# Kernel tuning notes

Hardware: AMD Instinct MI355X
Metric: run time of the kernel (lower is better)

Reference implementation:

```python
import jax, jax.numpy as jnp
import numpy as np

N, T, LH, HEADS, C, E = 100000, 24, 64, 4, 16, 1600000
NEG_SLOPE = 0.2  # PyG GATConv leaky_relu slope


def setup_inputs() -> dict:
    key = jax.random.key(0)
    ks = jax.random.split(key, 24)
    s = 0.05
    inp = {
        'input_tensor': jax.random.normal(ks[0], (N, T), jnp.float32),
        'edge_index': jax.random.randint(ks[1], (2, E), 0, N, jnp.int32),
        'edge_attr': jax.random.uniform(ks[2], (E, 1), jnp.float32),
        'knn_mask_short': jax.random.randint(ks[3], (E,), 0, 2, jnp.int32).astype(bool),
        # LSTM layer 1 (input_size=1): gate order i,f,g,o
        'W_ih1': jax.random.normal(ks[4], (4 * LH, 1), jnp.float32) * s,
        'W_hh1': jax.random.normal(ks[5], (4 * LH, LH), jnp.float32) * s,
        'b_ih1': jax.random.normal(ks[6], (4 * LH,), jnp.float32) * s,
        'b_hh1': jax.random.normal(ks[7], (4 * LH,), jnp.float32) * s,
        # LSTM layer 2 (input_size=LH)
        'W_ih2': jax.random.normal(ks[8], (4 * LH, LH), jnp.float32) * s,
        'W_hh2': jax.random.normal(ks[9], (4 * LH, LH), jnp.float32) * s,
        'b_ih2': jax.random.normal(ks[10], (4 * LH,), jnp.float32) * s,
        'b_hh2': jax.random.normal(ks[11], (4 * LH,), jnp.float32) * s,
        # GATConv params
        'gat_lin_w': jax.random.normal(ks[12], (HEADS * C, LH), jnp.float32) * s,
        'gat_lin_edge_w': jax.random.normal(ks[13], (HEADS * C, 1), jnp.float32) * s,
        'att_src': jax.random.normal(ks[14], (HEADS, C), jnp.float32) * s,
        'att_dst': jax.random.normal(ks[15], (HEADS, C), jnp.float32) * s,
        'att_edge': jax.random.normal(ks[16], (HEADS, C), jnp.float32) * s,
        'gat_bias': jax.random.normal(ks[17], (HEADS * C,), jnp.float32) * s,
        # final Linear
        'fc_w': jax.random.normal(ks[18], (1, HEADS * C), jnp.float32) * s,
        'fc_b': jax.random.normal(ks[19], (1,), jnp.float32) * s,
    }
    return inp


def _lstm_cell(x, h, c, W_ih, W_hh, b):
    z = x @ W_ih.T + h @ W_hh.T + b  # (N, 4H)
    i, f, g, o = jnp.split(z, 4, axis=-1)
    c = jax.nn.sigmoid(f) * c + jax.nn.sigmoid(i) * jnp.tanh(g)
    h = jax.nn.sigmoid(o) * jnp.tanh(c)
    return h, c


def reference(input_tensor, edge_index, edge_attr, knn_mask_short,
              W_ih1, W_hh1, b_ih1, b_hh1, W_ih2, W_hh2, b_ih2, b_hh2,
              gat_lin_w, gat_lin_edge_w, att_src, att_dst, att_edge, gat_bias,
              fc_w, fc_b):
    n = input_tensor.shape[0]
    # --- 2-layer LSTM over time, fused per-step (only final h2 needed) ---
    xs = input_tensor.T[:, :, None]  # (T, N, 1)
    b1 = b_ih1 + b_hh1
    b2 = b_ih2 + b_hh2
    z = jnp.zeros((n, LH), input_tensor.dtype)

    def step(carry, x_t):
        h1, c1, h2, c2 = carry
        h1, c1 = _lstm_cell(x_t, h1, c1, W_ih1, W_hh1, b1)
        h2, c2 = _lstm_cell(h1, h2, c2, W_ih2, W_hh2, b2)
        return (h1, c1, h2, c2), None

    (h1, c1, h2, c2), _ = jax.lax.scan(step, (z, z, z, z), xs)
    lstm_out = h2  # (N, LH): last time-step output of layer 2

    # --- GATConv (heads concat, edge_dim=1), eval mode (dropout off) ---
    x = (lstm_out @ gat_lin_w.T).reshape(n, HEADS, C)  # (N, H, C)
    a_src = jnp.einsum('nhc,hc->nh', x, att_src)
    a_dst = jnp.einsum('nhc,hc->nh', x, att_dst)
    src, dst = edge_index[0], edge_index[1]
    e = (edge_attr @ gat_lin_edge_w.T).reshape(-1, HEADS, C)  # (E, H, C)
    a_edge = jnp.einsum('ehc,hc->eh', e, att_edge)
    alpha = jax.nn.leaky_relu(a_src[src] + a_dst[dst] + a_edge, NEG_SLOPE)  # (E, H)
    # mask out non-'short' edges (equivalent to slicing them away)
    alpha = jnp.where(knn_mask_short[:, None], alpha, -1e30)
    amax = jax.ops.segment_max(alpha, dst, num_segments=n)  # (N, H)
    ex = jnp.exp(alpha - amax[dst]) * knn_mask_short[:, None].astype(alpha.dtype)
    denom = jax.ops.segment_sum(ex, dst, num_segments=n)  # (N, H)
    w = ex / jnp.maximum(denom[dst], 1e-16)  # (E, H) attention weights
    msg = x[src] * w[:, :, None]  # (E, H, C)
    out = jax.ops.segment_sum(msg, dst, num_segments=n).reshape(n, HEADS * C) + gat_bias

    out = jax.nn.elu(out)
    y = out @ fc_w.T + fc_b  # (N, 1)
    return y.reshape(n)
```

## Files before the change

kernel.cpp:

```cpp
#include <hip/hip_runtime.h>
#include <hip/hip_bf16.h>

#define T_STEPS 24
#define NSLOPE 0.2f
#define PITCH2 136
#define LOG2E 1.4426950408889634f

typedef _Float16 half8 __attribute__((ext_vector_type(8)));
typedef _Float16 half4_t __attribute__((ext_vector_type(4)));
typedef float floatx4 __attribute__((ext_vector_type(4)));

#if __has_builtin(__builtin_amdgcn_exp2f)
#define EXP2(x) __builtin_amdgcn_exp2f(x)
#else
#define EXP2(x) exp2f(x)
#endif
#define RCP(x) __builtin_amdgcn_rcpf(x)

#define ACT(A0,A1,A2,A3,CS,HP) {                                        \
    float i_ = RCP(1.f + EXP2(-(A0)));                                  \
    float f_ = RCP(1.f + EXP2(-(A1)));                                  \
    float gr = RCP(1.f + EXP2(-(A2)));                                  \
    float o_ = RCP(1.f + EXP2(-(A3)));                                  \
    float gs = fmaf(gr, 4.f*LOG2E, -2.f*LOG2E);                         \
    float cs = fmaf(f_, (CS), i_*gs);                                   \
    (CS) = cs;                                                          \
    float tc = fmaf(RCP(1.f + EXP2(-cs)), 2.f, -1.f);                   \
    (HP) = (_Float16)(o_*tc); }

__global__ __launch_bounds__(256) void prep_kernel(
    const float* __restrict__ W_ih1, const float* __restrict__ W_hh1,
    const float* __restrict__ b_ih1, const float* __restrict__ b_hh1,
    const float* __restrict__ W_ih2, const float* __restrict__ W_hh2,
    const float* __restrict__ b_ih2, const float* __restrict__ b_hh2,
    const float* __restrict__ glw, const float* __restrict__ glew,
    const float* __restrict__ atte, const unsigned char* __restrict__ mask_bytes,
    _Float16* __restrict__ W1F, _Float16* __restrict__ W2F, _Float16* __restrict__ W3F,
    float* __restrict__ b2P, float* __restrict__ ke, int* __restrict__ flag)
{
    int tid = blockIdx.x*blockDim.x + threadIdx.x;
    int nth = gridDim.x*blockDim.x;
    for (int idx = tid; idx < 24576; idx += nth){
        int b = idx & 7;
        int lane = (idx >> 3) & 63;
        int t2 = idx >> 9;
        int kt = t2 % 3;
        int t3 = t2 / 3;
        int m = t3 & 1, w = t3 >> 1;
        int row16 = lane & 15;
        int g = row16 & 3, cl = row16 >> 2;
        int row = g*64 + 8*w + 4*m + cl;
        float sc = (g == 2) ? 2.f*LOG2E : LOG2E;
        int k = (lane>>4)*8 + b;
        float val;
        if (kt < 2){ val = W_hh1[row*64 + 32*kt + k]; }
        else { val = (k == 0) ? W_ih1[row] : (k == 1) ? (b_ih1[row]+b_hh1[row]) : 0.f; }
        W1F[idx] = (_Float16)(val * sc);
    }
    for (int idx = tid; idx < 32768; idx += nth){
        int b = idx & 7;
        int lane = (idx >> 3) & 63;
        int kt = (idx >> 9) & 3;
        int t3 = idx >> 11;
        int m = t3 & 1, w = t3 >> 1;
        int row16 = lane & 15;
        int g = row16 & 3, cl = row16 >> 2;
        int row = g*64 + 8*w + 4*m + cl;
        float sc = (g == 2) ? 2.f*LOG2E : LOG2E;
        int k = 32*kt + (lane>>4)*8 + b;
        W2F[idx] = (_Float16)(((k < 64) ? W_ih2[row*64 + k] : W_hh2[row*64 + (k-64)]) * sc);
    }
    for (int idx = tid; idx < 4096; idx += nth){
        int b = idx & 7, t1 = idx >> 3; int lane = t1 & 63, t2 = t1 >> 6;
        int kt = t2 & 1, w = t2 >> 1;
        int row = 16*w + (lane & 15);
        W3F[idx] = (_Float16)glw[row*64 + 32*kt + (lane>>4)*8 + b];
    }
    for (int idx = tid; idx < 4096; idx += nth){
        int r = idx & 3;
        int lane = (idx >> 2) & 63;
        int m = (idx >> 8) & 1;
        int w = idx >> 9;
        int grp = lane >> 4;
        int row = r*64 + 8*w + 4*m + grp;
        float sc = (r == 2) ? 2.f*LOG2E : LOG2E;
        b2P[idx] = (b_ih2[row] + b_hh2[row]) * sc;
    }
    if (tid < 4){ float s = 0.f; for (int c = 0; c < 16; c++) s += atte[tid*16+c]*glew[tid*16+c]; ke[tid] = s; }
    if (tid == 0){ int nz = 0;
        for (int i = 0; i < 4096; i++){ if ((i&3) != 0 && mask_bytes[i] != 0) nz++; }
        *flag = (nz == 0) ? 1 : 0; }
}

__global__ __launch_bounds__(256) void count_kernel(
    const int* __restrict__ ei, const void* __restrict__ maskp, const int* __restrict__ flag,
    int* __restrict__ deg, int E)
{
    int e = blockIdx.x*256 + threadIdx.x;
    if (e >= E) return;
    bool m = (*flag) ? (((const int*)maskp)[e] != 0) : (((const unsigned char*)maskp)[e] != 0);
    if (!m) return;
    atomicAdd(deg + ei[E + e], 1);
}

__global__ __launch_bounds__(1024) void scan_kernel(
    const int* __restrict__ deg, int* __restrict__ offs, int* __restrict__ cursor, int nn)
{
    __shared__ int wsum[16];
    __shared__ int sbase;
    int lane = threadIdx.x & 63, wv = threadIdx.x >> 6;
    if (threadIdx.x == 0) sbase = 0;
    __syncthreads();
    for (int base = 0; base < nn; base += 4096){
        int i0 = base + (int)threadIdx.x*4;
        int4 v = make_int4(0,0,0,0);
        if (i0 + 3 < nn) v = *(const int4*)(deg + i0);
        else {
            if (i0   < nn) v.x = deg[i0];
            if (i0+1 < nn) v.y = deg[i0+1];
            if (i0+2 < nn) v.z = deg[i0+2];
            if (i0+3 < nn) v.w = deg[i0+3];
        }
        int s = v.x + v.y + v.z + v.w;
        int sc = s;
        #pragma unroll
        for (int o = 1; o < 64; o <<= 1){ int t = __shfl_up(sc, o); if (lane >= o) sc += t; }
        if (lane == 63) wsum[wv] = sc;
        __syncthreads();
        int wbase = 0, total = 0;
        #pragma unroll
        for (int k = 0; k < 16; k++){ int sk = wsum[k]; if (k < wv) wbase += sk; total += sk; }
        int excl = sbase + wbase + sc - s;
        if (i0 < nn){
            int e0 = excl, e1 = e0 + v.x, e2 = e1 + v.y, e3 = e2 + v.z;
            if (i0 + 3 < nn){
                *(int4*)(offs + i0)   = make_int4(e0,e1,e2,e3);
                *(int4*)(cursor + i0) = make_int4(e0,e1,e2,e3);
            } else {
                offs[i0] = e0; cursor[i0] = e0;
                if (i0+1 < nn){ offs[i0+1] = e1; cursor[i0+1] = e1; }
                if (i0+2 < nn){ offs[i0+2] = e2; cursor[i0+2] = e2; }
            }
        }
        __syncthreads();
        if (threadIdx.x == 0) sbase += total;
        __syncthreads();
    }
    if (threadIdx.x == 0) offs[nn] = sbase;
}

__global__ __launch_bounds__(256) void scatter_kernel(
    const int* __restrict__ ei, const float* __restrict__ ea, const void* __restrict__ maskp,
    const int* __restrict__ flag, int* __restrict__ cursor, int2* __restrict__ rec, int E)
{
    int e = blockIdx.x*256 + threadIdx.x;
    if (e >= E) return;
    bool m = (*flag) ? (((const int*)maskp)[e] != 0) : (((const unsigned char*)maskp)[e] != 0);
    if (!m) return;
    int d = ei[E + e];
    int pos = atomicAdd(cursor + d, 1);
    rec[pos] = make_int2(ei[e], __float_as_int(ea[e]));
}

#define MFMA16(A,B,C) __builtin_amdgcn_mfma_f32_16x16x32_f16((A),(B),(C),0,0,0)

__device__ __forceinline__ void lstm_step(
    const _Float16* RB, _Float16* WB, const _Float16* x_lds, int t,
    const half8 (&w1f)[2][3], const half8 (&w2f)[2][4], const floatx4 (&b2v)[2],
    float* c1s, float* c2s, int col, int grp, int wv)
{
    #pragma unroll
    for (int nt = 0; nt < 2; nt++){
        int node = nt*16 + col;
        half8 bf0 = *(const half8*)&RB[node*PITCH2 + grp*8];
        half8 bf1 = *(const half8*)&RB[node*PITCH2 + 32 + grp*8];
        half8 xb;
        #pragma unroll
        for (int b = 0; b < 8; b++) xb[b] = (_Float16)0.f;
        _Float16 xv = x_lds[node*26 + t];
        if (grp == 0){ xb[0] = xv; xb[1] = (_Float16)1.0f; }
        floatx4 aA = {0,0,0,0}, aB = {0,0,0,0};
        aA = MFMA16(w1f[0][0], bf0, aA);  aB = MFMA16(w1f[1][0], bf0, aB);
        aA = MFMA16(w1f[0][1], bf1, aA);  aB = MFMA16(w1f[1][1], bf1, aB);
        aA = MFMA16(w1f[0][2], xb,  aA);  aB = MFMA16(w1f[1][2], xb,  aB);
        _Float16 hA, hB;
        ACT(aA[0], aA[1], aA[2], aA[3], c1s[nt*2+0], hA);
        ACT(aB[0], aB[1], aB[2], aB[3], c1s[nt*2+1], hB);
        WB[node*PITCH2 + 8*wv + grp]     = hA;
        WB[node*PITCH2 + 8*wv + 4 + grp] = hB;
    }
    __syncthreads();
    #pragma unroll
    for (int nt = 0; nt < 2; nt++){
        int node = nt*16 + col;
        half8 bf0 = *(const half8*)&WB[node*PITCH2 + grp*8];
        half8 bf1 = *(const half8*)&WB[node*PITCH2 + 32 + grp*8];
        half8 bf2 = *(const half8*)&RB[node*PITCH2 + 64 + grp*8];
        half8 bf3 = *(const half8*)&RB[node*PITCH2 + 96 + grp*8];
        floatx4 aA = b2v[0], aB = b2v[1];
        aA = MFMA16(w2f[0][0], bf0, aA);  aB = MFMA16(w2f[1][0], bf0, aB);
        aA = MFMA16(w2f[0][1], bf1, aA);  aB = MFMA16(w2f[1][1], bf1, aB);
        aA = MFMA16(w2f[0][2], bf2, aA);  aB = MFMA16(w2f[1][2], bf2, aB);
        aA = MFMA16(w2f[0][3], bf3, aA);  aB = MFMA16(w2f[1][3], bf3, aB);
        _Float16 hA, hB;
        ACT(aA[0], aA[1], aA[2], aA[3], c2s[nt*2+0], hA);
        ACT(aB[0], aB[1], aB[2], aB[3], c2s[nt*2+1], hB);
        WB[node*PITCH2 + 64 + 8*wv + grp]     = hA;
        WB[node*PITCH2 + 64 + 8*wv + 4 + grp] = hB;
    }
    __syncthreads();
}

__global__ __launch_bounds__(512) void lstm_kernel(
    const float* __restrict__ x_in,
    const _Float16* __restrict__ W1F, const _Float16* __restrict__ W2F, const _Float16* __restrict__ W3F,
    const float* __restrict__ b2P,
    const float* __restrict__ atts, const float* __restrict__ attd,
    float* __restrict__ x_out, float* __restrict__ a_src, float* __restrict__ a_dst, int nn)
{
    __shared__ _Float16 hbuf0[32*PITCH2];
    __shared__ _Float16 hbuf1[32*PITCH2];
    __shared__ _Float16 x_lds[32*26];

    const int wv   = threadIdx.x >> 6;
    const int lane = threadIdx.x & 63;
    const int grp  = lane >> 4;
    const int col  = lane & 15;
    const int node0 = blockIdx.x * 32;

    for (int i = threadIdx.x; i < 32*T_STEPS; i += 512){
        int node = i / T_STEPS, t = i % T_STEPS;
        int nd = node0 + node;
        x_lds[node*26 + t] = (_Float16)((nd < nn) ? x_in[nd*T_STEPS + t] : 0.f);
    }
    for (int i = threadIdx.x; i < 32*PITCH2/2; i += 512) ((float*)hbuf0)[i] = 0.f;

    const half8* W1Fv = (const half8*)W1F;
    const half8* W2Fv = (const half8*)W2F;
    half8 w1f[2][3], w2f[2][4];
    floatx4 b2v[2];
    #pragma unroll
    for (int m = 0; m < 2; m++){
        #pragma unroll
        for (int kt = 0; kt < 3; kt++) w1f[m][kt] = W1Fv[((wv*2+m)*3+kt)*64 + lane];
        #pragma unroll
        for (int kt = 0; kt < 4; kt++) w2f[m][kt] = W2Fv[((wv*2+m)*4+kt)*64 + lane];
        b2v[m] = *(const floatx4*)&b2P[((wv*2+m)*64 + lane)*4];
    }

    float c1s[4], c2s[4];
    #pragma unroll
    for (int i = 0; i < 4; i++){ c1s[i] = 0.f; c2s[i] = 0.f; }

    __syncthreads();

    for (int t = 0; t < T_STEPS; t += 2){
        lstm_step(hbuf0, hbuf1, x_lds, t,   w1f, w2f, b2v, c1s, c2s, col, grp, wv);
        lstm_step(hbuf1, hbuf0, x_lds, t+1, w1f, w2f, b2v, c1s, c2s, col, grp, wv);
    }

    if (wv < 4){
        const half8* W3Fv = (const half8*)W3F;
        half8 w3f0 = W3Fv[(wv*2+0)*64 + lane];
        half8 w3f1 = W3Fv[(wv*2+1)*64 + lane];
        float asw[4], adw[4];
        #pragma unroll
        for (int r = 0; r < 4; r++){ int ch = 16*wv + grp*4 + r; asw[r] = atts[ch]; adw[r] = attd[ch]; }
        #pragma unroll
        for (int nt = 0; nt < 2; nt++){
            int node = nt*16 + col;
            int nd = node0 + node;
            floatx4 pa = {0,0,0,0};
            half8 bf0 = *(const half8*)&hbuf0[node*PITCH2 + 64 + grp*8];
            half8 bf1 = *(const half8*)&hbuf0[node*PITCH2 + 96 + grp*8];
            pa = MFMA16(w3f0, bf0, pa);
            pa = MFMA16(w3f1, bf1, pa);
            float s  = pa[0]*asw[0] + pa[1]*asw[1] + pa[2]*asw[2] + pa[3]*asw[3];
            float dv = pa[0]*adw[0] + pa[1]*adw[1] + pa[2]*adw[2] + pa[3]*adw[3];
            s  += __shfl_xor(s, 16);  s  += __shfl_xor(s, 32);
            dv += __shfl_xor(dv, 16); dv += __shfl_xor(dv, 32);
            if (nd < nn){
                *(float4*)(x_out + (size_t)nd*64 + 16*wv + grp*4) = make_float4(pa[0], pa[1], pa[2], pa[3]);
                if (grp == 0) a_src[nd*4 + wv] = s;
                else if (grp == 1) a_dst[nd*4 + wv] = dv;
            }
        }
    }
}

__global__ __launch_bounds__(256) void gather_kernel(
    const int2* __restrict__ rec, const int* __restrict__ offs,
    const float* __restrict__ a_src, const float* __restrict__ a_dst, const float* __restrict__ ke,
    const float* __restrict__ xf, const float* __restrict__ gbias,
    const float* __restrict__ fcw, const float* __restrict__ fcb,
    float* __restrict__ y, int nn)
{
    int wv = threadIdx.x >> 6, lane = threadIdx.x & 63;
    int node = blockIdx.x*4 + wv;
    if (node >= nn) return;
    int h = lane >> 4;
    float keh = ke[h];
    float adv = a_dst[4*node + h];
    int beg = offs[node], end = offs[node+1];
    float acc = 0.f, dacc = 0.f;
    int j = beg;
    for (; j + 1 < end; j += 2){
        int2 r0 = rec[j], r1 = rec[j+1];
        int s0 = r0.x, s1 = r1.x;
        float as0 = a_src[4*s0 + h], as1 = a_src[4*s1 + h];
        float x0 = xf[(size_t)s0*64 + lane], x1 = xf[(size_t)s1*64 + lane];
        float a0 = as0 + adv + __int_as_float(r0.y)*keh;
        float a1 = as1 + adv + __int_as_float(r1.y)*keh;
        a0 = a0 > 0.f ? a0 : NSLOPE*a0;
        a1 = a1 > 0.f ? a1 : NSLOPE*a1;
        float e0 = __expf(a0), e1 = __expf(a1);
        dacc += e0 + e1;
        acc = fmaf(e0, x0, acc);
        acc = fmaf(e1, x1, acc);
    }
    if (j < end){
        int2 r = rec[j];
        int s = r.x;
        float a = a_src[4*s + h] + adv + __int_as_float(r.y)*keh;
        a = a > 0.f ? a : NSLOPE*a;
        float ev = __expf(a);
        dacc += ev;
        acc = fmaf(ev, xf[(size_t)s*64 + lane], acc);
    }
    float v = acc * RCP(fmaxf(dacc, 1e-16f)) + gbias[lane];
    v = v > 0.f ? v : (__expf(v) - 1.f);
    float r2 = v * fcw[lane];
    #pragma unroll
    for (int off = 1; off < 64; off <<= 1) r2 += __shfl_xor(r2, off, 64);
    if (lane == 0) y[node] = r2 + fcb[0];
}

extern "C" void kernel_launch(void* const* d_in, const int* in_sizes, int n_in,
                              void* d_out, int out_size, void* d_ws, size_t ws_size,
                              hipStream_t stream)
{
    const float* x_in  = (const float*)d_in[0];
    const int*   ei    = (const int*)d_in[1];
    const float* ea    = (const float*)d_in[2];
    const void*  mask  = d_in[3];
    const float* W_ih1 = (const float*)d_in[4];
    const float* W_hh1 = (const float*)d_in[5];
    const float* b_ih1 = (const float*)d_in[6];
    const float* b_hh1 = (const float*)d_in[7];
    const float* W_ih2 = (const float*)d_in[8];
    const float* W_hh2 = (const float*)d_in[9];
    const float* b_ih2 = (const float*)d_in[10];
    const float* b_hh2 = (const float*)d_in[11];
    const float* glw   = (const float*)d_in[12];
    const float* glew  = (const float*)d_in[13];
    const float* atts  = (const float*)d_in[14];
    const float* attd  = (const float*)d_in[15];
    const float* atte  = (const float*)d_in[16];
    const float* gbias = (const float*)d_in[17];
    const float* fcw   = (const float*)d_in[18];
    const float* fcb   = (const float*)d_in[19];

    const int NN = in_sizes[0] / T_STEPS;
    const int E  = in_sizes[1] / 2;

    float* ws = (float*)d_ws;
    size_t o = 0;
    _Float16* W1F = (_Float16*)(ws + o); o += 24576/2;
    _Float16* W2F = (_Float16*)(ws + o); o += 32768/2;
    _Float16* W3F = (_Float16*)(ws + o); o += 4096/2;
    float* b2P = ws + o; o += 4096;
    float* ke  = ws + o; o += 64;
    int*  flag = (int*)(ws + o); o += 64;
    float* asrc= ws + o; o += (size_t)NN*4;
    float* adst= ws + o; o += (size_t)NN*4;
    float* xf  = ws + o; o += (size_t)NN*64;
    int* deg    = (int*)(ws + o); o += NN;
    int* offs   = (int*)(ws + o); o += NN + 64;
    int* cursor = (int*)(ws + o); o += NN;
    int2* rec   = (int2*)(ws + o); o += (size_t)E*2;

    hipMemsetAsync(deg, 0, (size_t)NN*sizeof(int), stream);

    prep_kernel<<<64, 256, 0, stream>>>(W_ih1, W_hh1, b_ih1, b_hh1, W_ih2, W_hh2, b_ih2, b_hh2,
                                        glw, glew, atte, (const unsigned char*)mask,
                                        W1F, W2F, W3F, b2P, ke, flag);
    count_kernel<<<(E + 255)/256, 256, 0, stream>>>(ei, mask, flag, deg, E);
    scan_kernel<<<1, 1024, 0, stream>>>(deg, offs, cursor, NN);
    scatter_kernel<<<(E + 255)/256, 256, 0, stream>>>(ei, ea, mask, flag, cursor, rec, E);
    lstm_kernel<<<(NN + 31)/32, 512, 0, stream>>>(x_in, W1F, W2F, W3F, b2P,
                                                  atts, attd, xf, asrc, adst, NN);
    gather_kernel<<<(NN + 3)/4, 256, 0, stream>>>(rec, offs, asrc, adst, ke, xf,
                                                  gbias, fcw, fcb, (float*)d_out, NN);
}
```

Before: 625.1 us.

## Skew LSTM layers into a wavefront pipeline with one barrier per step

```diff
diff --git a/kernel.cpp b/kernel.cpp
--- a/kernel.cpp
+++ b/kernel.cpp
@@ -7,7 +7,7 @@
 #define LOG2E 1.4426950408889634f
 
 typedef _Float16 half8 __attribute__((ext_vector_type(8)));
-typedef _Float16 half4_t __attribute__((ext_vector_type(4)));
+typedef _Float16 half2_t __attribute__((ext_vector_type(2)));
 typedef float floatx4 __attribute__((ext_vector_type(4)));
 
 #if __has_builtin(__builtin_amdgcn_exp2f)
@@ -27,6 +27,8 @@
     (CS) = cs;                                                          \
     float tc = fmaf(RCP(1.f + EXP2(-cs)), 2.f, -1.f);                   \
     (HP) = (_Float16)(o_*tc); }
+
+#define MFMA16(A,B,C) __builtin_amdgcn_mfma_f32_16x16x32_f16((A),(B),(C),0,0,0)
 
 __global__ __launch_bounds__(256) void prep_kernel(
     const float* __restrict__ W_ih1, const float* __restrict__ W_hh1,
@@ -49,7 +51,7 @@
         int m = t3 & 1, w = t3 >> 1;
         int row16 = lane & 15;
         int g = row16 & 3, cl = row16 >> 2;
-        int row = g*64 + 8*w + 4*m + cl;
+        int row = g*64 + 8*w + 2*cl + m;
         float sc = (g == 2) ? 2.f*LOG2E : LOG2E;
         int k = (lane>>4)*8 + b;
         float val;
@@ -65,7 +67,7 @@
         int m = t3 & 1, w = t3 >> 1;
         int row16 = lane & 15;
         int g = row16 & 3, cl = row16 >> 2;
-        int row = g*64 + 8*w + 4*m + cl;
+        int row = g*64 + 8*w + 2*cl + m;
         float sc = (g == 2) ? 2.f*LOG2E : LOG2E;
         int k = 32*kt + (lane>>4)*8 + b;
         W2F[idx] = (_Float16)(((k < 64) ? W_ih2[row*64 + k] : W_hh2[row*64 + (k-64)]) * sc);
@@ -82,7 +84,7 @@
         int m = (idx >> 8) & 1;
         int w = idx >> 9;
         int grp = lane >> 4;
-        int row = r*64 + 8*w + 4*m + grp;
+        int row = r*64 + 8*w + 2*grp + m;
         float sc = (r == 2) ? 2.f*LOG2E : LOG2E;
         b2P[idx] = (b_ih2[row] + b_hh2[row]) * sc;
     }
@@ -162,51 +164,94 @@
     rec[pos] = make_int2(ei[e], __float_as_int(ea[e]));
 }
 
-#define MFMA16(A,B,C) __builtin_amdgcn_mfma_f32_16x16x32_f16((A),(B),(C),0,0,0)
-
-__device__ __forceinline__ void lstm_step(
-    const _Float16* RB, _Float16* WB, const _Float16* x_lds, int t,
+__device__ __forceinline__ void lstm_phase(
+    _Float16* A, _Float16* B, const _Float16* x_lds, int tn,
     const half8 (&w1f)[2][3], const half8 (&w2f)[2][4], const floatx4 (&b2v)[2],
     float* c1s, float* c2s, int col, int grp, int wv)
 {
     #pragma unroll
     for (int nt = 0; nt < 2; nt++){
         int node = nt*16 + col;
-        half8 bf0 = *(const half8*)&RB[node*PITCH2 + grp*8];
-        half8 bf1 = *(const half8*)&RB[node*PITCH2 + 32 + grp*8];
+        half8 h1a = *(const half8*)&A[node*PITCH2 + grp*8];
+        half8 h1b = *(const half8*)&A[node*PITCH2 + 32 + grp*8];
+        half8 h2a = *(const half8*)&B[node*PITCH2 + 64 + grp*8];
+        half8 h2b = *(const half8*)&B[node*PITCH2 + 96 + grp*8];
+        floatx4 aA = b2v[0], aB = b2v[1];
+        aA = MFMA16(w2f[0][0], h1a, aA);  aB = MFMA16(w2f[1][0], h1a, aB);
+        aA = MFMA16(w2f[0][1], h1b, aA);  aB = MFMA16(w2f[1][1], h1b, aB);
+        aA = MFMA16(w2f[0][2], h2a, aA);  aB = MFMA16(w2f[1][2], h2a, aB);
+        aA = MFMA16(w2f[0][3], h2b, aA);  aB = MFMA16(w2f[1][3], h2b, aB);
         half8 xb;
         #pragma unroll
         for (int b = 0; b < 8; b++) xb[b] = (_Float16)0.f;
-        _Float16 xv = x_lds[node*26 + t];
+        _Float16 xv = x_lds[node*26 + tn];
         if (grp == 0){ xb[0] = xv; xb[1] = (_Float16)1.0f; }
-        floatx4 aA = {0,0,0,0}, aB = {0,0,0,0};
-        aA = MFMA16(w1f[0][0], bf0, aA);  aB = MFMA16(w1f[1][0], bf0, aB);
-        aA = MFMA16(w1f[0][1], bf1, aA);  aB = MFMA16(w1f[1][1], bf1, aB);
-        aA = MFMA16(w1f[0][2], xb,  aA);  aB = MFMA16(w1f[1][2], xb,  aB);
-        _Float16 hA, hB;
-        ACT(aA[0], aA[1], aA[2], aA[3], c1s[nt*2+0], hA);
-        ACT(aB[0], aB[1], aB[2], aB[3], c1s[nt*2+1], hB);
-        WB[node*PITCH2 + 8*wv + grp]     = hA;
-        WB[node*PITCH2 + 8*wv + 4 + grp] = hB;
-    }
-    __syncthreads();
-    #pragma unroll
-    for (int nt = 0; nt < 2; nt++){
-        int node = nt*16 + col;
-        half8 bf0 = *(const half8*)&WB[node*PITCH2 + grp*8];
-        half8 bf1 = *(const half8*)&WB[node*PITCH2 + 32 + grp*8];
-        half8 bf2 = *(const half8*)&RB[node*PITCH2 + 64 + grp*8];
-        half8 bf3 = *(const half8*)&RB[node*PITCH2 + 96 + grp*8];
-        floatx4 aA = b2v[0], aB = b2v[1];
-        aA = MFMA16(w2f[0][0], bf0, aA);  aB = MFMA16(w2f[1][0], bf0, aB);
-        aA = MFMA16(w2f[0][1], bf1, aA);  aB = MFMA16(w2f[1][1], bf1, aB);
-        aA = MFMA16(w2f[0][2], bf2, aA);  aB = MFMA16(w2f[1][2], bf2, aB);
-        aA = MFMA16(w2f[0][3], bf3, aA);  aB = MFMA16(w2f[1][3], bf3, aB);
+        floatx4 cA = {0,0,0,0}, cB = {0,0,0,0};
+        cA = MFMA16(w1f[0][0], h1a, cA);  cB = MFMA16(w1f[1][0], h1a, cB);
+        cA = MFMA16(w1f[0][1], h1b, cA);  cB = MFMA16(w1f[1][1], h1b, cB);
+        cA = MFMA16(w1f[0][2], xb,  cA);  cB = MFMA16(w1f[1][2], xb,  cB);
         _Float16 hA, hB;
         ACT(aA[0], aA[1], aA[2], aA[3], c2s[nt*2+0], hA);
         ACT(aB[0], aB[1], aB[2], aB[3], c2s[nt*2+1], hB);
-        WB[node*PITCH2 + 64 + 8*wv + grp]     = hA;
-        WB[node*PITCH2 + 64 + 8*wv + 4 + grp] = hB;
+        { half2_t hh; hh[0] = hA; hh[1] = hB;
+          *(half2_t*)&A[node*PITCH2 + 64 + 8*wv + 2*grp] = hh; }
+        ACT(cA[0], cA[1], cA[2], cA[3], c1s[nt*2+0], hA);
+        ACT(cB[0], cB[1], cB[2], cB[3], c1s[nt*2+1], hB);
+        { half2_t hh; hh[0] = hA; hh[1] = hB;
+          *(half2_t*)&B[node*PITCH2 + 8*wv + 2*grp] = hh; }
+    }
+    __syncthreads();
+}
+
+__device__ __forceinline__ void lstm_l1only(
+    const _Float16* R, _Float16* W, const _Float16* x_lds,
+    const half8 (&w1f)[2][3], float* c1s, int col, int grp, int wv)
+{
+    #pragma unroll
+    for (int nt = 0; nt < 2; nt++){
+        int node = nt*16 + col;
+        half8 h1a = *(const half8*)&R[node*PITCH2 + grp*8];
+        half8 h1b = *(const half8*)&R[node*PITCH2 + 32 + grp*8];
+        half8 xb;
+        #pragma unroll
+        for (int b = 0; b < 8; b++) xb[b] = (_Float16)0.f;
+        _Float16 xv = x_lds[node*26 + 0];
+        if (grp == 0){ xb[0] = xv; xb[1] = (_Float16)1.0f; }
+        floatx4 cA = {0,0,0,0}, cB = {0,0,0,0};
+        cA = MFMA16(w1f[0][0], h1a, cA);  cB = MFMA16(w1f[1][0], h1a, cB);
+        cA = MFMA16(w1f[0][1], h1b, cA);  cB = MFMA16(w1f[1][1], h1b, cB);
+        cA = MFMA16(w1f[0][2], xb,  cA);  cB = MFMA16(w1f[1][2], xb,  cB);
+        _Float16 hA, hB;
+        ACT(cA[0], cA[1], cA[2], cA[3], c1s[nt*2+0], hA);
+        ACT(cB[0], cB[1], cB[2], cB[3], c1s[nt*2+1], hB);
+        half2_t hh; hh[0] = hA; hh[1] = hB;
+        *(half2_t*)&W[node*PITCH2 + 8*wv + 2*grp] = hh;
+    }
+    __syncthreads();
+}
+
+__device__ __forceinline__ void lstm_l2only(
+    _Float16* H1, const _Float16* H2,
+    const half8 (&w2f)[2][4], const floatx4 (&b2v)[2],
+    float* c2s, int col, int grp, int wv)
+{
+    #pragma unroll
+    for (int nt = 0; nt < 2; nt++){
+        int node = nt*16 + col;
+        half8 h1a = *(const half8*)&H1[node*PITCH2 + grp*8];
+        half8 h1b = *(const half8*)&H1[node*PITCH2 + 32 + grp*8];
+        half8 h2a = *(const half8*)&H2[node*PITCH2 + 64 + grp*8];
+        half8 h2b = *(const half8*)&H2[node*PITCH2 + 96 + grp*8];
+        floatx4 aA = b2v[0], aB = b2v[1];
+        aA = MFMA16(w2f[0][0], h1a, aA);  aB = MFMA16(w2f[1][0], h1a, aB);
+        aA = MFMA16(w2f[0][1], h1b, aA);  aB = MFMA16(w2f[1][1], h1b, aB);
+        aA = MFMA16(w2f[0][2], h2a, aA);  aB = MFMA16(w2f[1][2], h2a, aB);
+        aA = MFMA16(w2f[0][3], h2b, aA);  aB = MFMA16(w2f[1][3], h2b, aB);
+        _Float16 hA, hB;
+        ACT(aA[0], aA[1], aA[2], aA[3], c2s[nt*2+0], hA);
+        ACT(aB[0], aB[1], aB[2], aB[3], c2s[nt*2+1], hB);
+        half2_t hh; hh[0] = hA; hh[1] = hB;
+        *(half2_t*)&H1[node*PITCH2 + 64 + 8*wv + 2*grp] = hh;
     }
     __syncthreads();
 }
@@ -254,10 +299,13 @@
 
     __syncthreads();
 
-    for (int t = 0; t < T_STEPS; t += 2){
-        lstm_step(hbuf0, hbuf1, x_lds, t,   w1f, w2f, b2v, c1s, c2s, col, grp, wv);
-        lstm_step(hbuf1, hbuf0, x_lds, t+1, w1f, w2f, b2v, c1s, c2s, col, grp, wv);
-    }
+    lstm_l1only(hbuf0, hbuf1, x_lds, w1f, c1s, col, grp, wv);
+    for (int k = 0; k < 11; k++){
+        lstm_phase(hbuf1, hbuf0, x_lds, 2*k+1, w1f, w2f, b2v, c1s, c2s, col, grp, wv);
+        lstm_phase(hbuf0, hbuf1, x_lds, 2*k+2, w1f, w2f, b2v, c1s, c2s, col, grp, wv);
+    }
+    lstm_phase(hbuf1, hbuf0, x_lds, 23, w1f, w2f, b2v, c1s, c2s, col, grp, wv);
+    lstm_l2only(hbuf0, hbuf1, w2f, b2v, c2s, col, grp, wv);
 
     if (wv < 4){
         const half8* W3Fv = (const half8*)W3F;
```

Result: slower. 683.1 us (+9.3%).
